# Optimization experiments

Measured on AMD Instinct MI355X. Metric: run time of the kernel, lower is better.

## Reference

```python
import jax, jax.numpy as jnp
import numpy as np

N_STATES = 21


def setup_inputs() -> dict:
    key = jax.random.key(0)
    ks = jax.random.split(key, 12)
    N_pulses, B = 128, 8192
    u = lambda k, shape, lo, hi: jax.random.uniform(k, shape, jnp.float32, lo, hi)
    return {
        "flip_angles": u(ks[0], (N_pulses,), 0.0, jnp.pi / 2),  # rad
        "phases": u(ks[1], (N_pulses,), 0.0, 2 * jnp.pi),
        "T1f": u(ks[2], (B,), 800.0, 1500.0),   # ms
        "T2f": u(ks[3], (B,), 50.0, 100.0),
        "T1b": u(ks[4], (B,), 200.0, 400.0),
        "T2b": u(ks[5], (B,), 8.0, 20.0),
        "kf": u(ks[6], (B,), 1.0, 5.0),
        "kb": u(ks[7], (B,), 1.0, 5.0),
        "B0": jax.random.normal(ks[8], (B,), jnp.float32) * 20.0,  # Hz
        "B1": u(ks[9], (B,), 0.8, 1.2),
        "wf": u(ks[10], (B,), 0.85, 0.95),
        "wb": u(ks[11], (B,), 0.05, 0.15),
        "TR": 10,
        "TE": 5,
    }


def _simulate(flip_angles, phases, T1f, T2f, T1b, T2b, kf, kb, B0, B1, wf, wb, TR):
    B = T1f.shape[0]
    col = lambda v: v.astype(jnp.float32)[:, None]  # (B,1) for broadcast over states
    T1f, T2f, T1b, T2b = col(T1f), col(T2f), col(T1b), col(T2b)
    kf, kb, B0, B1, wf, wb = col(kf), col(kb), col(B0), col(B1), col(wf), col(wb)
    TR = jnp.float32(TR)
    E1f, E2f = jnp.exp(-TR / T1f), jnp.exp(-TR / T2f)
    E1b, E2b = jnp.exp(-TR / T1b), jnp.exp(-TR / T2b)
    phi = 2.0 * jnp.pi * B0 * TR / 1000.0
    b0_p = jnp.exp(1j * phi).astype(jnp.complex64)   # (B,1)
    b0_m = jnp.conj(b0_p)
    dt = TR / 1000.0

    czeros = jnp.zeros((B, N_STATES), jnp.complex64)
    Zf0 = jnp.zeros((B, N_STATES), jnp.float32).at[:, 0].set(wf[:, 0])
    Zb0 = jnp.zeros((B, N_STATES), jnp.float32).at[:, 0].set(wb[:, 0])
    carry0 = (czeros, czeros, Zf0, czeros, czeros, Zb0)

    def shift(Fp, Fm, Z):
        Fp = jnp.roll(Fp, 1, axis=1).at[:, 0].set(0)
        Fm = jnp.roll(Fm, -1, axis=1).at[:, -1].set(0)
        Z = jnp.roll(Z, 1, axis=1).at[:, 0].set(0)
        return Fp, Fm, Z

    def step(carry, fa_ph):
        Fpf, Fmf, Zf, Fpb, Fmb, Zb = carry
        fa, ph = fa_ph
        # --- relax + exchange ---
        Fpf, Fmf = Fpf * E2f, Fmf * E2f
        Fpb, Fmb = Fpb * E2b, Fmb * E2b
        dZf = (-kf * Zf + kb * Zb) * dt
        dZb = (-kb * Zb + kf * Zf) * dt
        Zf_t1 = (Zf * E1f).at[:, 0].add((1.0 - E1f[:, 0]) * wf[:, 0])
        Zb_t1 = (Zb * E1b).at[:, 0].add((1.0 - E1b[:, 0]) * wb[:, 0])
        Zf, Zb = Zf_t1 + dZf, Zb_t1 + dZb
        # --- B0 precession (both pools) ---
        Fpf, Fmf = Fpf * b0_p, Fmf * b0_m
        Fpb, Fmb = Fpb * b0_p, Fmb * b0_m
        # --- RF pulse (free pool only, as in the torch code) ---
        alpha = fa * B1  # (B,1)
        ca, sa = jnp.cos(alpha / 2), jnp.sin(alpha / 2)
        eib = jnp.exp(1j * ph).astype(jnp.complex64)
        emib = jnp.conj(eib)
        Fpf_n = ca**2 * Fpf + sa**2 * jnp.conj(Fmf) * eib**2 + 1j * ca * sa * (Zf * eib)
        Fmf_n = sa**2 * jnp.conj(Fpf) * emib**2 + ca**2 * Fmf - 1j * ca * sa * (Zf * emib)
        Zf_n = (-1j * sa * ca * (Fpf * emib - Fmf * eib) + (ca**2 - sa**2) * Zf).real
        Fpf, Fmf, Zf = Fpf_n, Fmf_n, Zf_n
        # --- EPG shift (both pools) ---
        Fpf, Fmf, Zf = shift(Fpf, Fmf, Zf)
        Fpb, Fmb, Zb = shift(Fpb, Fmb, Zb)
        carry = (Fpf, Fmf, Zf, Fpb, Fmb, Zb)
        # real-valued packed state: (B, n_states, 10)
        out = jnp.stack([Fpf.real, Fpf.imag, Fmf.real, Fmf.imag, Zf,
                         Fpb.real, Fpb.imag, Fmb.real, Fmb.imag, Zb], axis=-1)
        return carry, out

    xs = (flip_angles.astype(jnp.float32), phases.astype(jnp.float32))
    _, states = jax.lax.scan(step, carry0, xs)
    return states  # (N_pulses, B, n_states, 10)


def reference(flip_angles, phases, T1f, T2f, T1b, T2b, kf, kb, B0, B1, wf, wb, TR, TE):
    # TE is accepted (matches the torch signature) but unused by the simulation.
    return _simulate(flip_angles, phases, T1f, T2f, T1b, T2b, kf, kb, B0, B1, wf, wb, TR)
```

## Files before the change

kernel.cpp:

```cpp
#include <hip/hip_runtime.h>
#include <math.h>

#define NSTATES 21
#define NPULSES 128
#define BATCH   8192

__global__ __launch_bounds__(256) void epg_mt_kernel(
    const float* __restrict__ fa_arr,
    const float* __restrict__ ph_arr,
    const float* __restrict__ T1f, const float* __restrict__ T2f,
    const float* __restrict__ T1b, const float* __restrict__ T2b,
    const float* __restrict__ kfp, const float* __restrict__ kbp,
    const float* __restrict__ B0p, const float* __restrict__ B1p,
    const float* __restrict__ wfp, const float* __restrict__ wbp,
    const int*   __restrict__ TRp,
    float* __restrict__ out)
{
    const int lane = threadIdx.x & 63;
    const int wid  = (int)((blockIdx.x * blockDim.x + threadIdx.x) >> 6);
    const int g    = lane / 21;
    const int s    = lane - g * 21;
    const int b    = wid * 3 + g;
    if (g >= 3 || b >= BATCH) return;

    const float tr  = (float)TRp[0];
    const float dt  = tr * 0.001f;
    const float E1f = expf(-tr / T1f[b]);
    const float E2f = expf(-tr / T2f[b]);
    const float E1b = expf(-tr / T1b[b]);
    const float kfdt = kfp[b] * dt;
    const float kbdt = kbp[b] * dt;
    const float phi  = 6.28318530717958647692f * B0p[b] * dt;
    const float b0c  = cosf(phi), b0s = sinf(phi);
    const float wfv  = wfp[b], wbv = wbp[b];
    const float add0f = (s == 0) ? (1.0f - E1f) * wfv : 0.0f;
    const float add0b = (s == 0) ? (1.0f - E1b) * wbv : 0.0f;
    const float b1   = B1p[b];

    float Fpr = 0.f, Fpi = 0.f, Fmr = 0.f, Fmi = 0.f;
    float Zf = (s == 0) ? wfv : 0.f;
    float Zb = (s == 0) ? wbv : 0.f;

    float* op = out + (size_t)b * (NSTATES * 10) + (size_t)s * 10;
    const size_t pstride = (size_t)BATCH * NSTATES * 10;

    for (int p = 0; p < NPULSES; ++p) {
        const float fa = fa_arr[p];
        const float ph = ph_arr[p];

        Fpr *= E2f; Fpi *= E2f; Fmr *= E2f; Fmi *= E2f;
        const float dZf = kbdt * Zb - kfdt * Zf;
        const float dZb = kfdt * Zf - kbdt * Zb;
        const float nZf1 = fmaf(Zf, E1f, add0f) + dZf;
        const float nZb1 = fmaf(Zb, E1b, add0b) + dZb;
        Zf = nZf1; Zb = nZb1;

        {
            const float r  = Fpr * b0c - Fpi * b0s;
            const float i_ = Fpr * b0s + Fpi * b0c;
            const float r2 = Fmr * b0c + Fmi * b0s;
            const float i2 = Fmi * b0c - Fmr * b0s;
            Fpr = r; Fpi = i_; Fmr = r2; Fmi = i2;
        }

        const float half = 0.5f * fa * b1;
        const float ca = __cosf(half), sa = __sinf(half);
        const float cph = __cosf(ph), sph = __sinf(ph);
        const float ca2 = ca * ca, sa2 = sa * sa, casa = ca * sa;
        const float cd  = ca2 - sa2;
        const float e2c = cph * cph - sph * sph;
        const float e2s = 2.f * cph * sph;
        const float t1r = Fmr * e2c + Fmi * e2s;
        const float t1i = Fmr * e2s - Fmi * e2c;
        const float t2r = Fpr * e2c - Fpi * e2s;
        const float t2i = -(Fpr * e2s) - Fpi * e2c;
        const float zc = Zf * cph, zs = Zf * sph;
        const float nFpr = ca2 * Fpr + sa2 * t1r - casa * zs;
        const float nFpi = ca2 * Fpi + sa2 * t1i + casa * zc;
        const float nFmr = sa2 * t2r + ca2 * Fmr - casa * zs;
        const float nFmi = sa2 * t2i + ca2 * Fmi - casa * zc;
        const float nZf = casa * ((Fpi * cph - Fpr * sph) - (Fmi * cph + Fmr * sph)) + cd * Zf;
        Fpr = nFpr; Fpi = nFpi; Fmr = nFmr; Fmi = nFmi; Zf = nZf;

        const float sFpr = __shfl_up(Fpr, 1);
        const float sFpi = __shfl_up(Fpi, 1);
        const float sZf  = __shfl_up(Zf, 1);
        const float sZb  = __shfl_up(Zb, 1);
        const float sFmr = __shfl_down(Fmr, 1);
        const float sFmi = __shfl_down(Fmi, 1);
        const bool s0 = (s == 0), sE = (s == NSTATES - 1);
        Fpr = s0 ? 0.f : sFpr;
        Fpi = s0 ? 0.f : sFpi;
        Zf  = s0 ? 0.f : sZf;
        Zb  = s0 ? 0.f : sZb;
        Fmr = sE ? 0.f : sFmr;
        Fmi = sE ? 0.f : sFmi;

        float2* o2 = (float2*)op;
        o2[0] = make_float2(Fpr, Fpi);
        o2[1] = make_float2(Fmr, Fmi);
        o2[2] = make_float2(Zf, 0.f);
        o2[3] = make_float2(0.f, 0.f);
        o2[4] = make_float2(0.f, Zb);
        op += pstride;
    }
}

extern "C" void kernel_launch(void* const* d_in, const int* in_sizes, int n_in,
                              void* d_out, int out_size, void* d_ws, size_t ws_size,
                              hipStream_t stream) {
    const float* fa  = (const float*)d_in[0];
    const float* ph  = (const float*)d_in[1];
    const float* T1f = (const float*)d_in[2];
    const float* T2f = (const float*)d_in[3];
    const float* T1b = (const float*)d_in[4];
    const float* T2b = (const float*)d_in[5];
    const float* kf  = (const float*)d_in[6];
    const float* kb  = (const float*)d_in[7];
    const float* B0  = (const float*)d_in[8];
    const float* B1  = (const float*)d_in[9];
    const float* wf  = (const float*)d_in[10];
    const float* wb  = (const float*)d_in[11];
    const int*   TR  = (const int*)d_in[12];
    float* out = (float*)d_out;

    const int waves  = (BATCH + 2) / 3;
    const int blocks = (waves + 3) / 4;
    epg_mt_kernel<<<blocks, 256, 0, stream>>>(fa, ph, T1f, T2f, T1b, T2b,
                                              kf, kb, B0, B1, wf, wb, TR, out);
}
```

Measured before the change: 211.1 us.

## Stage per-pulse outputs in LDS and write coalesced 16-byte vector stores

Each wave now handles 2 batch elements laid out as 32-lane halves, instead of 3 elements packed into 21-lane groups. It buffers the state records for 4 pulses in LDS, then writes them to global memory as contiguous float4 stores across the whole wave. This replaces the previous scattered float2 stores, which had a 40-byte stride per lane, and is meant to improve write coalescing on an output-bandwidth-bound kernel. The cost is lower lane utilisation (42 of 64 lanes active in compute), extra LDS traffic, and reliance on a manual lgkmcnt wait with no barrier, which is valid only because each wave touches its own LDS region.

```diff
diff --git a/kernel.cpp b/kernel.cpp
--- a/kernel.cpp
+++ b/kernel.cpp
@@ -4,8 +4,15 @@
 #define NSTATES 21
 #define NPULSES 128
 #define BATCH   8192
+#define CHUNK   4
+#define WPB     8
+#define EPW     2
+#define EPB     (WPB * EPW)
+#define RECF    (NSTATES * 10)
 
-__global__ __launch_bounds__(256) void epg_mt_kernel(
+typedef float v4f __attribute__((ext_vector_type(4)));
+
+__global__ __launch_bounds__(512) void epg_mt_kernel(
     const float* __restrict__ fa_arr,
     const float* __restrict__ ph_arr,
     const float* __restrict__ T1f, const float* __restrict__ T2f,
@@ -16,12 +23,19 @@
     const int*   __restrict__ TRp,
     float* __restrict__ out)
 {
-    const int lane = threadIdx.x & 63;
-    const int wid  = (int)((blockIdx.x * blockDim.x + threadIdx.x) >> 6);
-    const int g    = lane / 21;
-    const int s    = lane - g * 21;
-    const int b    = wid * 3 + g;
-    if (g >= 3 || b >= BATCH) return;
+    __shared__ __attribute__((aligned(16))) float lds[WPB][CHUNK * EPW * RECF];
+
+    const int tid  = threadIdx.x;
+    const int wv   = tid >> 6;
+    const int lane = tid & 63;
+    const int g    = lane >> 5;
+    const int s    = lane & 31;
+    const bool valid = (s < NSTATES);
+    const int b    = blockIdx.x * EPB + wv * EPW + g;
+
+    float* ldsw = lds[wv];
+    for (int i = lane; i < CHUNK * EPW * RECF; i += 64)
+        ldsw[i] = 0.f;
 
     const float tr  = (float)TRp[0];
     const float dt  = tr * 0.001f;
@@ -41,20 +55,16 @@
     float Zf = (s == 0) ? wfv : 0.f;
     float Zb = (s == 0) ? wbv : 0.f;
 
-    float* op = out + (size_t)b * (NSTATES * 10) + (size_t)s * 10;
-    const size_t pstride = (size_t)BATCH * NSTATES * 10;
+    const size_t pstride = (size_t)BATCH * RECF;
+    float* outw = out + ((size_t)blockIdx.x * EPB + wv * EPW) * RECF;
 
-    for (int p = 0; p < NPULSES; ++p) {
-        const float fa = fa_arr[p];
-        const float ph = ph_arr[p];
-
+    auto step = [&](float fa, float ph) {
         Fpr *= E2f; Fpi *= E2f; Fmr *= E2f; Fmi *= E2f;
         const float dZf = kbdt * Zb - kfdt * Zf;
         const float dZb = kfdt * Zf - kbdt * Zb;
         const float nZf1 = fmaf(Zf, E1f, add0f) + dZf;
         const float nZb1 = fmaf(Zb, E1b, add0b) + dZb;
         Zf = nZf1; Zb = nZb1;
-
         {
             const float r  = Fpr * b0c - Fpi * b0s;
             const float i_ = Fpr * b0s + Fpi * b0c;
@@ -62,7 +72,6 @@
             const float i2 = Fmi * b0c - Fmr * b0s;
             Fpr = r; Fpi = i_; Fmr = r2; Fmi = i2;
         }
-
         const float half = 0.5f * fa * b1;
         const float ca = __cosf(half), sa = __sinf(half);
         const float cph = __cosf(ph), sph = __sinf(ph);
@@ -81,7 +90,6 @@
         const float nFmi = sa2 * t2i + ca2 * Fmi - casa * zc;
         const float nZf = casa * ((Fpi * cph - Fpr * sph) - (Fmi * cph + Fmr * sph)) + cd * Zf;
         Fpr = nFpr; Fpi = nFpi; Fmr = nFmr; Fmi = nFmi; Zf = nZf;
-
         const float sFpr = __shfl_up(Fpr, 1);
         const float sFpi = __shfl_up(Fpi, 1);
         const float sZf  = __shfl_up(Zf, 1);
@@ -95,14 +103,33 @@
         Zb  = s0 ? 0.f : sZb;
         Fmr = sE ? 0.f : sFmr;
         Fmi = sE ? 0.f : sFmi;
+    };
 
-        float2* o2 = (float2*)op;
-        o2[0] = make_float2(Fpr, Fpi);
-        o2[1] = make_float2(Fmr, Fmi);
-        o2[2] = make_float2(Zf, 0.f);
-        o2[3] = make_float2(0.f, 0.f);
-        o2[4] = make_float2(0.f, Zb);
-        op += pstride;
+    for (int pc = 0; pc < NPULSES; pc += CHUNK) {
+        #pragma unroll
+        for (int cp = 0; cp < CHUNK; ++cp) {
+            step(fa_arr[pc + cp], ph_arr[pc + cp]);
+            if (valid) {
+                float* dst = ldsw + (cp * EPW + g) * RECF + s * 10;
+                ((float2*)dst)[0] = make_float2(Fpr, Fpi);
+                ((float2*)dst)[1] = make_float2(Fmr, Fmi);
+                dst[4] = Zf;
+                dst[9] = Zb;
+            }
+        }
+        asm volatile("s_waitcnt lgkmcnt(0)" ::: "memory");
+
+        #pragma unroll
+        for (int cp = 0; cp < CHUNK; ++cp) {
+            const v4f* Ls = (const v4f*)(ldsw + cp * EPW * RECF);
+            v4f* og = (v4f*)(outw + (size_t)(pc + cp) * pstride);
+            #pragma unroll
+            for (int i = 0; i < 2; ++i) {
+                int idx = lane + i * 64;
+                if (idx < (EPW * RECF) / 4)
+                    og[idx] = Ls[idx];
+            }
+        }
     }
 }
 
@@ -124,8 +151,7 @@
     const int*   TR  = (const int*)d_in[12];
     float* out = (float*)d_out;
 
-    const int waves  = (BATCH + 2) / 3;
-    const int blocks = (waves + 3) / 4;
-    epg_mt_kernel<<<blocks, 256, 0, stream>>>(fa, ph, T1f, T2f, T1b, T2b,
-                                              kf, kb, B0, B1, wf, wb, TR, out);
+    const int blocks = BATCH / EPB;
+    epg_mt_kernel<<<blocks, WPB * 64, 0, stream>>>(fa, ph, T1f, T2f, T1b, T2b,
+                                                   kf, kb, B0, B1, wf, wb, TR, out);
 }
```

Result: slower. 220.2 us (+4.3%).

## Stage per-batch output records in LDS for coalesced contiguous global stores

Applied to the files above, without the earlier changes.

Each wavefront now handles one batch element instead of three, and writes its 210-float state record per pulse into LDS, then copies it to global memory as contiguous float2 stores across lanes. The old path had each lane issue five strided float2 stores, ten floats apart. The aim is to coalesce writes in this store-bound kernel. In exchange, 43 of 64 lanes sit idle during compute, there are 2.67x more waves, and each pulse adds LDS traffic. No barrier is placed between the LDS write and read, which relies on the wave running in lockstep.

```diff
diff --git a/kernel.cpp b/kernel.cpp
--- a/kernel.cpp
+++ b/kernel.cpp
@@ -4,8 +4,11 @@
 #define NSTATES 21
 #define NPULSES 128
 #define BATCH   8192
+#define EPB     4
+#define RECF    (NSTATES * 10)
+#define RECPAD  224
 
-__global__ __launch_bounds__(256) void epg_mt_kernel(
+__global__ __launch_bounds__(256, 8) void epg_mt_kernel(
     const float* __restrict__ fa_arr,
     const float* __restrict__ ph_arr,
     const float* __restrict__ T1f, const float* __restrict__ T2f,
@@ -16,12 +19,18 @@
     const int*   __restrict__ TRp,
     float* __restrict__ out)
 {
-    const int lane = threadIdx.x & 63;
-    const int wid  = (int)((blockIdx.x * blockDim.x + threadIdx.x) >> 6);
-    const int g    = lane / 21;
-    const int s    = lane - g * 21;
-    const int b    = wid * 3 + g;
-    if (g >= 3 || b >= BATCH) return;
+    __shared__ float lds[EPB][RECPAD];
+
+    const int tid  = threadIdx.x;
+    const int wv   = tid >> 6;
+    const int lane = tid & 63;
+    const int s    = lane;
+    const bool active = (lane < NSTATES);
+    const int b    = blockIdx.x * EPB + wv;
+
+    float* myrec = lds[wv];
+    for (int i = lane; i < RECPAD; i += 64)
+        myrec[i] = 0.f;
 
     const float tr  = (float)TRp[0];
     const float dt  = tr * 0.001f;
@@ -41,8 +50,10 @@
     float Zf = (s == 0) ? wfv : 0.f;
     float Zb = (s == 0) ? wbv : 0.f;
 
-    float* op = out + (size_t)b * (NSTATES * 10) + (size_t)s * 10;
-    const size_t pstride = (size_t)BATCH * NSTATES * 10;
+    const size_t pstride2 = (size_t)BATCH * RECF / 2;
+    float2* outw = (float2*)(out + (size_t)b * RECF);
+    const float2* myrec2 = (const float2*)myrec;
+    const bool has2 = lane < (RECF / 2 - 64);
 
     for (int p = 0; p < NPULSES; ++p) {
         const float fa = fa_arr[p];
@@ -96,13 +107,20 @@
         Fmr = sE ? 0.f : sFmr;
         Fmi = sE ? 0.f : sFmi;
 
-        float2* o2 = (float2*)op;
-        o2[0] = make_float2(Fpr, Fpi);
-        o2[1] = make_float2(Fmr, Fmi);
-        o2[2] = make_float2(Zf, 0.f);
-        o2[3] = make_float2(0.f, 0.f);
-        o2[4] = make_float2(0.f, Zb);
-        op += pstride;
+        if (active) {
+            float* dst = myrec + s * 10;
+            ((float2*)dst)[0] = make_float2(Fpr, Fpi);
+            ((float2*)dst)[1] = make_float2(Fmr, Fmi);
+            dst[4] = Zf;
+            dst[9] = Zb;
+        }
+
+        float2 v0 = myrec2[lane];
+        float2 v1;
+        if (has2) v1 = myrec2[lane + 64];
+        float2* og = outw + (size_t)p * pstride2;
+        og[lane] = v0;
+        if (has2) og[lane + 64] = v1;
     }
 }
 
@@ -124,8 +142,7 @@
     const int*   TR  = (const int*)d_in[12];
     float* out = (float*)d_out;
 
-    const int waves  = (BATCH + 2) / 3;
-    const int blocks = (waves + 3) / 4;
+    const int blocks = BATCH / EPB;
     epg_mt_kernel<<<blocks, 256, 0, stream>>>(fa, ph, T1f, T2f, T1b, T2b,
                                               kf, kb, B0, B1, wf, wb, TR, out);
 }
```

New measurement: 227.0 us. 7.5% more time.
